# Kernel optimization log

Measured on AMD Instinct MI355X. Metric: run time of the kernel, lower is better.

## Reference

```python
import jax, jax.numpy as jnp
import numpy as np

N_NODES = 50000
IN_FEATS, HID_FEATS, OUT_FEATS, HEADS = 128, 32, 64, 4
NEG_SLOPE = 0.2
EPS = 1e-16


def gat_conv(x, src, dst, W, att_src, att_dst, bias, heads, out_ch, concat):
    """PyG-style GATConv. src/dst: [E] (self-loops already included).
    W: [in, heads*out_ch]; att_src/att_dst: [heads, out_ch]; bias: [heads*out_ch] or [out_ch].
    """
    n = x.shape[0]
    xw = (x @ W).reshape(n, heads, out_ch)                     # [N,H,C]
    a_src = (xw * att_src).sum(-1)                             # [N,H]
    a_dst = (xw * att_dst).sum(-1)                             # [N,H]
    e = jax.nn.leaky_relu(a_src[src] + a_dst[dst], NEG_SLOPE)  # [E,H]
    # segment softmax over incoming edges of each destination node
    m = jax.ops.segment_max(e, dst, num_segments=n)
    e = jnp.exp(e - m[dst])
    denom = jax.ops.segment_sum(e, dst, num_segments=n)
    alpha = e / (denom[dst] + EPS)                             # [E,H]
    out = jax.ops.segment_sum(alpha[:, :, None] * xw[src], dst, num_segments=n)  # [N,H,C]
    out = out.reshape(n, heads * out_ch) if concat else out.mean(axis=1)
    return out + bias


def setup_inputs() -> dict:
    key = jax.random.key(0)
    ks = jax.random.split(key, 10)
    E = 1600000
    x = jax.random.normal(ks[0], (N_NODES, IN_FEATS), dtype=jnp.float32)
    edge_index = jax.random.randint(ks[1], (2, E), 0, N_NODES, dtype=jnp.int64)
    s1 = 1.0 / np.sqrt(IN_FEATS)
    W1 = jax.random.uniform(ks[2], (IN_FEATS, HEADS * HID_FEATS), jnp.float32, -s1, s1)
    att_src1 = jax.random.normal(ks[3], (HEADS, HID_FEATS), dtype=jnp.float32) * 0.1
    att_dst1 = jax.random.normal(ks[4], (HEADS, HID_FEATS), dtype=jnp.float32) * 0.1
    b1 = jnp.zeros((HEADS * HID_FEATS,), jnp.float32)
    s2 = 1.0 / np.sqrt(HEADS * HID_FEATS)
    W2 = jax.random.uniform(ks[5], (HEADS * HID_FEATS, OUT_FEATS), jnp.float32, -s2, s2)
    att_src2 = jax.random.normal(ks[6], (1, OUT_FEATS), dtype=jnp.float32) * 0.1
    att_dst2 = jax.random.normal(ks[7], (1, OUT_FEATS), dtype=jnp.float32) * 0.1
    b2 = jnp.zeros((OUT_FEATS,), jnp.float32)
    return {"x": x, "edge_index": edge_index, "W1": W1, "att_src1": att_src1,
            "att_dst1": att_dst1, "b1": b1, "W2": W2, "att_src2": att_src2,
            "att_dst2": att_dst2, "b2": b2}


def reference(x, edge_index, W1, att_src1, att_dst1, b1, W2, att_src2, att_dst2, b2):
    n = x.shape[0]
    loops = jnp.arange(n, dtype=edge_index.dtype)
    src = jnp.concatenate([edge_index[0], loops])
    dst = jnp.concatenate([edge_index[1], loops])
    h = gat_conv(x, src, dst, W1, att_src1, att_dst1, b1, HEADS, HID_FEATS, True)
    h = jax.nn.elu(h)
    h = gat_conv(h, src, dst, W2, att_src2, att_dst2, b2, 1, OUT_FEATS, False)
    return h.mean(axis=0)
```

## Files before the change

kernel.cpp:

```cpp
#include <hip/hip_runtime.h>
#include <math.h>

#define N_NODES 50000
#define SN      N_NODES
#define E_RAW   1600000
#define TE      (E_RAW + N_NODES)
#define TEP     (TE + 16 * N_NODES)
#define F_IN    128
#define H1      4
#define F1      128
#define F2      64
#define NEG_SLOPE 0.2f
#define EPS_F   1e-16f
#define XPAD    136
#define LOG2E   1.4426950408889634f

#define NBINS   196
#define NBLK_A  128
#define EPB     ((TE + NBLK_A - 1) / NBLK_A)
#define MM_BLOCKS (N_NODES / 16)

typedef float vf2 __attribute__((ext_vector_type(2)));
typedef short short8 __attribute__((ext_vector_type(8)));
typedef float f32x4 __attribute__((ext_vector_type(4)));

__device__ __forceinline__ unsigned short f2bf(float f) {
    unsigned u = __float_as_uint(f);
    return (unsigned short)((u + 0x7fffu + ((u >> 16) & 1u)) >> 16);
}
__device__ __forceinline__ unsigned char f2fp8(float f) {
    int p = __builtin_amdgcn_cvt_pk_fp8_f32(f, f, 0, false);
    return (unsigned char)(p & 0xff);
}
__device__ __forceinline__ vf2 fp8lo(unsigned u) {
    return __builtin_amdgcn_cvt_pk_f32_fp8((int)u, false);
}
__device__ __forceinline__ vf2 fp8hi(unsigned u) {
    return __builtin_amdgcn_cvt_pk_f32_fp8((int)u, true);
}
__device__ __forceinline__ vf2 pkfma(float w, vf2 a, vf2 c) {
#if __has_builtin(__builtin_elementwise_fma)
    vf2 wv = {w, w};
    return __builtin_elementwise_fma(wv, a, c);
#else
    c.x = fmaf(w, a.x, c.x);
    c.y = fmaf(w, a.y, c.y);
    return c;
#endif
}
__device__ __forceinline__ float fexp2(float x) {
#if __has_builtin(__builtin_amdgcn_exp2f)
    return __builtin_amdgcn_exp2f(x);
#else
    return exp2f(x);
#endif
}

__global__ __launch_bounds__(256) void k_prep(const float* __restrict__ W1,
                                              const float* __restrict__ W2,
                                              unsigned short* __restrict__ w1t,
                                              unsigned short* __restrict__ w2t,
                                              float* __restrict__ a1s,
                                              float* __restrict__ a2s,
                                              unsigned* __restrict__ xw1row,
                                              unsigned* __restrict__ xw2row) {
    int idx = blockIdx.x * 256 + threadIdx.x;
    if (idx < 16384) {
        int c = idx >> 7, k = idx & 127;
        w1t[idx] = f2bf(W1[k * F1 + c]);
    } else {
        int j = idx - 16384;
        int c = j >> 7, k = j & 127;
        w2t[j] = f2bf(W2[k * F2 + c]);
    }
    if (blockIdx.x == 0 && threadIdx.x < H1) a1s[SN * H1 + threadIdx.x] = -1e30f;
    if (blockIdx.x == 0 && threadIdx.x == H1) a2s[SN] = -1e30f;
    if (blockIdx.x == 1) {
        if (threadIdx.x < 32) xw1row[threadIdx.x] = 0u;
        else if (threadIdx.x < 48) xw2row[threadIdx.x - 32] = 0u;
    }
}

__global__ __launch_bounds__(256) void k_l1_mm_hist(
    const float* __restrict__ x, const unsigned short* __restrict__ w1t,
    const float* __restrict__ atts, const float* __restrict__ attd,
    unsigned char* __restrict__ xwf8, float* __restrict__ a1s, float* __restrict__ a1d,
    const int* __restrict__ ei, int* __restrict__ cnt) {
    __shared__ __align__(16) unsigned short wls[F1 * XPAD];
    __shared__ __align__(16) unsigned short xs[16 * XPAD];
    const int t = threadIdx.x;
    if (blockIdx.x >= MM_BLOCKS) {
        int* hist = (int*)wls;
        const int blk = blockIdx.x - MM_BLOCKS;
        for (int i = t; i < NBINS; i += 256) hist[i] = 0;
        __syncthreads();
        const int e0 = blk * EPB, e1 = min(TE, e0 + EPB);
        for (int e = e0 + t; e < e1; e += 256) {
            int d = (e < E_RAW) ? ei[E_RAW + e] : (e - E_RAW);
            atomicAdd(&hist[d >> 8], 1);
        }
        __syncthreads();
        for (int i = t; i < NBINS; i += 256) cnt[i * NBLK_A + blk] = hist[i];
        return;
    }
    const int n0 = blockIdx.x * 16;
    {
        const float4* src = (const float4*)(x + (size_t)n0 * F_IN);
#pragma unroll
        for (int i = 0; i < 2; ++i) {
            int idx = t + 256 * i;
            float4 v = src[idx];
            int row = idx >> 5;
            int col = (idx & 31) * 4;
            ushort4 o = { f2bf(v.x), f2bf(v.y), f2bf(v.z), f2bf(v.w) };
            *(ushort4*)(xs + row * XPAD + col) = o;
        }
        const uint4* wsrc = (const uint4*)w1t;
#pragma unroll
        for (int i = 0; i < 8; ++i) {
            int idx = t + 256 * i;
            uint4 v = wsrc[idx];
            int row = idx >> 4;
            int col = (idx & 15) * 8;
            *(uint4*)(wls + row * XPAD + col) = v;
        }
    }
    __syncthreads();
    const int w = t >> 6;
    const int lane = t & 63;
    const int quad = lane >> 4;
    const int ncol = lane & 15;
    const int ch0 = w * 32;
    const unsigned short* arow = xs + ncol * XPAD;
    const unsigned short* brow0 = wls + (ch0 + ncol) * XPAD;
    const unsigned short* brow1 = brow0 + 16 * XPAD;
    f32x4 acc0 = {0.f, 0.f, 0.f, 0.f}, acc1 = {0.f, 0.f, 0.f, 0.f};
#pragma unroll
    for (int s = 0; s < 4; ++s) {
        int kb = s * 32 + quad * 8;
        short8 a  = *(const short8*)(arow + kb);
        short8 b0 = *(const short8*)(brow0 + kb);
        short8 b1 = *(const short8*)(brow1 + kb);
        acc0 = __builtin_amdgcn_mfma_f32_16x16x32_bf16(a, b0, acc0, 0, 0, 0);
        acc1 = __builtin_amdgcn_mfma_f32_16x16x32_bf16(a, b1, acc1, 0, 0, 0);
    }
    const int ch = ch0 + ncol;
    const float as0 = atts[ch] * LOG2E, as1 = atts[ch + 16] * LOG2E;
    const float ad0 = attd[ch] * LOG2E, ad1 = attd[ch + 16] * LOG2E;
#pragma unroll
    for (int reg = 0; reg < 4; ++reg) {
        const int n = n0 + quad * 4 + reg;
        float v0 = acc0[reg], v1 = acc1[reg];
        xwf8[(size_t)n * F1 + ch] = f2fp8(v0);
        xwf8[(size_t)n * F1 + ch + 16] = f2fp8(v1);
        float ps = fmaf(v0, as0, v1 * as1);
        float pd = fmaf(v0, ad0, v1 * ad1);
#pragma unroll
        for (int off = 1; off < 16; off <<= 1) {
            ps += __shfl_xor(ps, off);
            pd += __shfl_xor(pd, off);
        }
        if (ncol == 0) {
            a1s[n * H1 + w] = ps;
            a1d[n * H1 + w] = pd;
        }
    }
}

__global__ __launch_bounds__(1024) void k_binscan(int* __restrict__ cnt,
                                                  int* __restrict__ bstart) {
    __shared__ int bt[NBINS];
    const int t = threadIdx.x, lane = t & 63, w = t >> 6;
    for (int bin = w; bin < NBINS; bin += 16) {
        int c0 = cnt[bin * NBLK_A + 2 * lane];
        int c1 = cnt[bin * NBLK_A + 2 * lane + 1];
        int s = c0 + c1;
        int incl = s;
#pragma unroll
        for (int off = 1; off < 64; off <<= 1) {
            int u = __shfl_up(incl, off, 64);
            if (lane >= off) incl += u;
        }
        int excl = incl - s;
        cnt[bin * NBLK_A + 2 * lane] = excl;
        cnt[bin * NBLK_A + 2 * lane + 1] = excl + c0;
        if (lane == 63) bt[bin] = incl;
    }
    __syncthreads();
    if (w == 0) {
        int v[4]; int s = 0;
#pragma unroll
        for (int j = 0; j < 4; ++j) {
            int i = 4 * lane + j;
            v[j] = (i < NBINS) ? bt[i] : 0;
            s += v[j];
        }
        int incl = s;
#pragma unroll
        for (int off = 1; off < 64; off <<= 1) {
            int u = __shfl_up(incl, off, 64);
            if (lane >= off) incl += u;
        }
        int run = incl - s;
#pragma unroll
        for (int j = 0; j < 4; ++j) {
            int i = 4 * lane + j;
            if (i < NBINS) bstart[i] = run;
            run += v[j];
        }
        if (lane == 63) bstart[NBINS] = TE;
    }
}

__global__ __launch_bounds__(256) void k_scatter_coarse(const int* __restrict__ ei,
                                                        const int* __restrict__ cnt,
                                                        const int* __restrict__ bstart,
                                                        unsigned* __restrict__ cbuf) {
    __shared__ int cur[NBINS];
    const int t = threadIdx.x, blk = blockIdx.x;
    for (int i = t; i < NBINS; i += 256) cur[i] = cnt[i * NBLK_A + blk] + bstart[i];
    __syncthreads();
    const int e0 = blk * EPB, e1 = min(TE, e0 + EPB);
    for (int e = e0 + t; e < e1; e += 256) {
        int s, d;
        if (e < E_RAW) { s = ei[e]; d = ei[E_RAW + e]; }
        else { s = e - E_RAW; d = s; }
        int pos = atomicAdd(&cur[d >> 8], 1);
        cbuf[pos] = ((unsigned)(d & 255) << 16) | (unsigned)s;
    }
}

__global__ __launch_bounds__(256) void k_fine_hist(const unsigned* __restrict__ cbuf,
                                                   const int* __restrict__ bstart,
                                                   int* __restrict__ deg) {
    __shared__ int hist[256];
    const int t = threadIdx.x, b = blockIdx.x;
    hist[t] = 0;
    __syncthreads();
    const int i0 = bstart[b], i1 = bstart[b + 1];
    for (int i = i0 + t; i < i1; i += 256) atomicAdd(&hist[cbuf[i] >> 16], 1);
    __syncthreads();
    const int d = b * 256 + t;
    if (d < N_NODES) deg[d] = hist[t];
}

__global__ __launch_bounds__(1024) void k_scan1(const int* __restrict__ deg,
                                                int* __restrict__ incl, int* __restrict__ bsum) {
    int t = threadIdx.x, g = blockIdx.x;
    int idx = g * 1024 + t;
    int v = (idx < N_NODES) ? ((deg[idx] + 15) & ~15) : 0;
    int lane = t & 63, w = t >> 6;
#pragma unroll
    for (int off = 1; off < 64; off <<= 1) {
        int u = __shfl_up(v, off, 64);
        if (lane >= off) v += u;
    }
    __shared__ int ws[16];
    if (lane == 63) ws[w] = v;
    __syncthreads();
    if (w == 0 && lane < 16) {
        int s = ws[lane];
#pragma unroll
        for (int off = 1; off < 16; off <<= 1) {
            int u = __shfl_up(s, off, 16);
            if (lane >= off) s += u;
        }
        ws[lane] = s;
    }
    __syncthreads();
    if (w > 0) v += ws[w - 1];
    if (idx < N_NODES) incl[idx] = v;
    if (t == 1023) bsum[g] = v;
}

__global__ __launch_bounds__(1024) void k_scan3(const int* __restrict__ incl,
                                                const int* __restrict__ bsum,
                                                int* __restrict__ rowstart) {
    __shared__ int soff;
    const int t = threadIdx.x;
    if (t < 64) {
        int v = (t < blockIdx.x) ? bsum[t] : 0;
#pragma unroll
        for (int off = 32; off >= 1; off >>= 1) v += __shfl_xor(v, off, 64);
        if (t == 0) soff = v;
    }
    __syncthreads();
    const int idx = blockIdx.x * 1024 + t;
    if (idx < N_NODES) rowstart[idx + 1] = incl[idx] + soff;
    if (idx == 0) rowstart[0] = 0;
}

__global__ __launch_bounds__(256) void k_build_csr(const unsigned* __restrict__ cbuf,
                                                   const int* __restrict__ bstart,
                                                   const int* __restrict__ rowstart,
                                                   const int* __restrict__ deg,
                                                   int* __restrict__ csr) {
    __shared__ int cur[256];
    const int t = threadIdx.x, b = blockIdx.x;
    const int d = b * 256 + t;
    cur[t] = (d < N_NODES) ? rowstart[d] : 0;
    __syncthreads();
    const int i0 = bstart[b], i1 = bstart[b + 1];
    for (int i = i0 + t; i < i1; i += 256) {
        unsigned v = cbuf[i];
        int pos = atomicAdd(&cur[v >> 16], 1);
        csr[pos] = (int)(v & 0xffffu);
    }
    __syncthreads();
    if (d < N_NODES) {
        const int pend = rowstart[d] + ((deg[d] + 15) & ~15);
        for (int i = cur[t]; i < pend; ++i) csr[i] = SN;
    }
}

__global__ __launch_bounds__(256) void k_l1_gather(
    const int* __restrict__ rowstart, const int* __restrict__ csr,
    const int* __restrict__ deg, const float* __restrict__ a1s,
    const float* __restrict__ a1d, const unsigned* __restrict__ xwu,
    const float* __restrict__ b1, float* __restrict__ h1) {
    const int lane = threadIdx.x & 63;
    const int wid = threadIdx.x >> 6;
    const int n = blockIdx.x * 4 + wid;
    if (n >= N_NODES) return;
    const int rs = rowstart[n];
    const int nb16 = (deg[n] + 15) >> 4;
    const int half = lane >> 5;
    const int sub = lane & 31;
    const int h = sub >> 3;
    const float adh = a1d[n * H1 + h];
    const int4* c4 = (const int4*)(csr + rs);
    const int eoff = half * 8 + (sub & 7);
    const int wbase = half * 32 + (h << 3);
    vf2 f01 = {0.f, 0.f}, f23 = {0.f, 0.f};
    float den_l = 0.f;
    for (int b = 0; b < nb16; ++b) {
        const int i0 = 4 * b + 2 * half;
        int4 sA = c4[i0], sB = c4[i0 + 1];
        int se = csr[rs + 16 * b + eoff];
        unsigned u0 = xwu[sA.x * 32 + sub], u1 = xwu[sA.y * 32 + sub];
        unsigned u2 = xwu[sA.z * 32 + sub], u3 = xwu[sA.w * 32 + sub];
        unsigned u4 = xwu[sB.x * 32 + sub], u5 = xwu[sB.y * 32 + sub];
        unsigned u6 = xwu[sB.z * 32 + sub], u7 = xwu[sB.w * 32 + sub];
        float sv = a1s[se * H1 + h] + adh;
        float we = fexp2(fmaxf(sv, NEG_SLOPE * sv));
        den_l += we;
        float w0 = __shfl(we, wbase + 0), w1 = __shfl(we, wbase + 1);
        float w2 = __shfl(we, wbase + 2), w3 = __shfl(we, wbase + 3);
        float w4 = __shfl(we, wbase + 4), w5 = __shfl(we, wbase + 5);
        float w6 = __shfl(we, wbase + 6), w7 = __shfl(we, wbase + 7);
        f01 = pkfma(w0, fp8lo(u0), f01); f23 = pkfma(w0, fp8hi(u0), f23);
        f01 = pkfma(w1, fp8lo(u1), f01); f23 = pkfma(w1, fp8hi(u1), f23);
        f01 = pkfma(w2, fp8lo(u2), f01); f23 = pkfma(w2, fp8hi(u2), f23);
        f01 = pkfma(w3, fp8lo(u3), f01); f23 = pkfma(w3, fp8hi(u3), f23);
        f01 = pkfma(w4, fp8lo(u4), f01); f23 = pkfma(w4, fp8hi(u4), f23);
        f01 = pkfma(w5, fp8lo(u5), f01); f23 = pkfma(w5, fp8hi(u5), f23);
        f01 = pkfma(w6, fp8lo(u6), f01); f23 = pkfma(w6, fp8hi(u6), f23);
        f01 = pkfma(w7, fp8lo(u7), f01); f23 = pkfma(w7, fp8hi(u7), f23);
    }
    float f0 = f01.x, f1 = f01.y, f2v = f23.x, f3 = f23.y;
    f0 += __shfl_xor(f0, 32);
    f1 += __shfl_xor(f1, 32);
    f2v += __shfl_xor(f2v, 32);
    f3 += __shfl_xor(f3, 32);
    den_l += __shfl_xor(den_l, 1);
    den_l += __shfl_xor(den_l, 2);
    den_l += __shfl_xor(den_l, 4);
    den_l += __shfl_xor(den_l, 32);
    if (half == 0) {
        const float inv = 1.f / (den_l + EPS_F);
        float4 bb = ((const float4*)b1)[sub];
        float o0 = fmaf(f0, inv, bb.x);
        float o1 = fmaf(f1, inv, bb.y);
        float o2 = fmaf(f2v, inv, bb.z);
        float o3 = fmaf(f3, inv, bb.w);
        o0 = o0 > 0.f ? o0 : expm1f(o0);
        o1 = o1 > 0.f ? o1 : expm1f(o1);
        o2 = o2 > 0.f ? o2 : expm1f(o2);
        o3 = o3 > 0.f ? o3 : expm1f(o3);
        ((float4*)h1)[(size_t)n * 32 + sub] = make_float4(o0, o1, o2, o3);
    }
}

__global__ __launch_bounds__(256) void k_l2_mm(
    const float* __restrict__ h1, const unsigned short* __restrict__ w2t,
    const float* __restrict__ atts, const float* __restrict__ attd,
    unsigned char* __restrict__ xwf8, float* __restrict__ a2s, float* __restrict__ a2d) {
    __shared__ __align__(16) unsigned short wls[F2 * XPAD];
    __shared__ __align__(16) unsigned short xs[16 * XPAD];
    __shared__ float parts[16][4], partd[16][4];
    const int t = threadIdx.x;
    const int n0 = blockIdx.x * 16;
    {
        const float4* src = (const float4*)(h1 + (size_t)n0 * F1);
#pragma unroll
        for (int i = 0; i < 2; ++i) {
            int idx = t + 256 * i;
            float4 v = src[idx];
            int row = idx >> 5;
            int col = (idx & 31) * 4;
            ushort4 o = { f2bf(v.x), f2bf(v.y), f2bf(v.z), f2bf(v.w) };
            *(ushort4*)(xs + row * XPAD + col) = o;
        }
        const uint4* wsrc = (const uint4*)w2t;
#pragma unroll
        for (int i = 0; i < 4; ++i) {
            int idx = t + 256 * i;
            uint4 v = wsrc[idx];
            int row = idx >> 4;
            int col = (idx & 15) * 8;
            *(uint4*)(wls + row * XPAD + col) = v;
        }
    }
    __syncthreads();
    const int w = t >> 6;
    const int lane = t & 63;
    const int quad = lane >> 4;
    const int ncol = lane & 15;
    const int ch0 = w * 16;
    const unsigned short* arow = xs + ncol * XPAD;
    const unsigned short* brow = wls + (ch0 + ncol) * XPAD;
    f32x4 acc = {0.f, 0.f, 0.f, 0.f};
#pragma unroll
    for (int s = 0; s < 4; ++s) {
        int kb = s * 32 + quad * 8;
        short8 a = *(const short8*)(arow + kb);
        short8 b = *(const short8*)(brow + kb);
        acc = __builtin_amdgcn_mfma_f32_16x16x32_bf16(a, b, acc, 0, 0, 0);
    }
    const int ch = ch0 + ncol;
    const float asv = atts[ch] * LOG2E, adv = attd[ch] * LOG2E;
#pragma unroll
    for (int reg = 0; reg < 4; ++reg) {
        const int m = quad * 4 + reg;
        float v = acc[reg];
        xwf8[(size_t)(n0 + m) * F2 + ch] = f2fp8(v);
        float ps = v * asv, pd = v * adv;
#pragma unroll
        for (int off = 1; off < 16; off <<= 1) {
            ps += __shfl_xor(ps, off);
            pd += __shfl_xor(pd, off);
        }
        if (ncol == 0) { parts[m][w] = ps; partd[m][w] = pd; }
    }
    __syncthreads();
    if (t < 16) {
        a2s[n0 + t] = (parts[t][0] + parts[t][1]) + (parts[t][2] + parts[t][3]);
        a2d[n0 + t] = (partd[t][0] + partd[t][1]) + (partd[t][2] + partd[t][3]);
    }
}

__global__ __launch_bounds__(256) void k_l2_gather(
    const int* __restrict__ rowstart, const int* __restrict__ csr,
    const int* __restrict__ deg, const float* __restrict__ a2s,
    const float* __restrict__ a2d, const unsigned* __restrict__ xwu,
    float* __restrict__ h2) {
    const int lane = threadIdx.x & 63;
    const int wid = threadIdx.x >> 6;
    const int n = blockIdx.x * 4 + wid;
    if (n >= N_NODES) return;
    const int rs = rowstart[n];
    const int nb16 = (deg[n] + 15) >> 4;
    const int q = lane >> 4;
    const int sub = lane & 15;
    const float adv = a2d[n];
    const int4* c4 = (const int4*)(csr + rs);
    vf2 f01 = {0.f, 0.f}, f23 = {0.f, 0.f};
    float den_l = 0.f;
    for (int b = 0; b < nb16; ++b) {
        int4 s4 = c4[4 * b + q];
        int se = csr[rs + 16 * b + sub];
        unsigned u0 = xwu[s4.x * 16 + sub], u1 = xwu[s4.y * 16 + sub];
        unsigned u2 = xwu[s4.z * 16 + sub], u3 = xwu[s4.w * 16 + sub];
        float sv = a2s[se] + adv;
        float we = fexp2(fmaxf(sv, NEG_SLOPE * sv));
        den_l += we;
        float w0 = __shfl(we, 4 * q + 0), w1 = __shfl(we, 4 * q + 1);
        float w2 = __shfl(we, 4 * q + 2), w3 = __shfl(we, 4 * q + 3);
        f01 = pkfma(w0, fp8lo(u0), f01); f23 = pkfma(w0, fp8hi(u0), f23);
        f01 = pkfma(w1, fp8lo(u1), f01); f23 = pkfma(w1, fp8hi(u1), f23);
        f01 = pkfma(w2, fp8lo(u2), f01); f23 = pkfma(w2, fp8hi(u2), f23);
        f01 = pkfma(w3, fp8lo(u3), f01); f23 = pkfma(w3, fp8hi(u3), f23);
    }
    float f0 = f01.x, f1 = f01.y, f2v = f23.x, f3 = f23.y;
#pragma unroll
    for (int off = 16; off <= 32; off <<= 1) {
        f0 += __shfl_xor(f0, off);
        f1 += __shfl_xor(f1, off);
        f2v += __shfl_xor(f2v, off);
        f3 += __shfl_xor(f3, off);
    }
#pragma unroll
    for (int off = 1; off <= 32; off <<= 1) den_l += __shfl_xor(den_l, off);
    if (lane < 16) {
        const float inv = 1.f / (0.25f * den_l + EPS_F);
        ((float4*)h2)[(size_t)n * 16 + sub] =
            make_float4(f0 * inv, f1 * inv, f2v * inv, f3 * inv);
    }
}

#define MEAN_BLOCKS 256
__global__ __launch_bounds__(256) void k_mean(const float* __restrict__ h2,
                                              double* __restrict__ accum) {
    const int t = threadIdx.x;
    const int c = t & 63;
    double acc = 0.0;
    const size_t total = (size_t)N_NODES * F2;
    for (size_t idx = (size_t)blockIdx.x * 256 + t; idx < total; idx += (size_t)MEAN_BLOCKS * 256)
        acc += (double)h2[idx];
    __shared__ double red[256];
    red[t] = acc;
    __syncthreads();
    if (t < 64) {
        double v = red[t] + red[t + 64] + red[t + 128] + red[t + 192];
        atomicAdd(&accum[c], v);
    }
}

__global__ void k_final(const double* __restrict__ accum, const float* __restrict__ b2,
                        float* __restrict__ out) {
    int t = threadIdx.x;
    if (t < F2) out[t] = (float)(accum[t] * (1.0 / (double)N_NODES)) + b2[t];
}

extern "C" void kernel_launch(void* const* d_in, const int* in_sizes, int n_in,
                              void* d_out, int out_size, void* d_ws, size_t ws_size,
                              hipStream_t stream) {
    (void)in_sizes; (void)n_in; (void)out_size; (void)ws_size;
    const float* x   = (const float*)d_in[0];
    const int*   ei  = (const int*)d_in[1];
    const float* W1  = (const float*)d_in[2];
    const float* as1 = (const float*)d_in[3];
    const float* ad1 = (const float*)d_in[4];
    const float* b1  = (const float*)d_in[5];
    const float* W2  = (const float*)d_in[6];
    const float* as2 = (const float*)d_in[7];
    const float* ad2 = (const float*)d_in[8];
    const float* b2  = (const float*)d_in[9];
    float* out = (float*)d_out;

    char* ws = (char*)d_ws;
    size_t off = 0;
    auto alloc = [&](size_t bytes) -> void* {
        void* p = ws + off;
        off += (bytes + 255) & ~(size_t)255;
        return p;
    };
    unsigned char*  xw1f8 = (unsigned char*)alloc((size_t)(N_NODES + 1) * F1);
    float* h1       = (float*)alloc((size_t)N_NODES * F1 * 4);
    unsigned char*  xw2f8 = (unsigned char*)alloc((size_t)(N_NODES + 1) * F2);
    float* h2       = (float*)alloc((size_t)N_NODES * F2 * 4);
    unsigned short* w1t = (unsigned short*)alloc((size_t)F1 * F1 * 2);
    unsigned short* w2t = (unsigned short*)alloc((size_t)F2 * F1 * 2);
    float* a1s      = (float*)alloc((size_t)(N_NODES + 1) * H1 * 4);
    float* a1d      = (float*)alloc((size_t)N_NODES * H1 * 4);
    float* a2s      = (float*)alloc((size_t)(N_NODES + 1) * 4);
    float* a2d      = (float*)alloc((size_t)N_NODES * 4);
    int*   deg      = (int*)alloc((size_t)N_NODES * 4);
    unsigned* cbuf  = (unsigned*)alloc((size_t)TE * 4);
    int*   cnt      = (int*)alloc((size_t)NBINS * NBLK_A * 4);
    int*   bstart   = (int*)alloc((size_t)(NBINS + 1) * 4);
    int*   rowstart = (int*)alloc((size_t)(N_NODES + 1) * 4);
    int*   csr      = (int*)alloc((size_t)TEP * 4);
    int*   incl     = (int*)alloc((size_t)N_NODES * 4);
    int*   bsum     = (int*)alloc(64 * 4);
    double* accum   = (double*)alloc(F2 * 8);

    const int nscan = (N_NODES + 1023) / 1024;
    const int nwave4 = (N_NODES + 3) / 4;

    hipMemsetAsync(accum, 0, F2 * 8, stream);
    k_prep<<<96, 256, 0, stream>>>(W1, W2, w1t, w2t, a1s, a2s,
                                   (unsigned*)(xw1f8 + (size_t)SN * F1),
                                   (unsigned*)(xw2f8 + (size_t)SN * F2));
    k_l1_mm_hist<<<MM_BLOCKS + NBLK_A, 256, 0, stream>>>(x, w1t, as1, ad1, xw1f8, a1s, a1d, ei, cnt);
    k_binscan<<<1, 1024, 0, stream>>>(cnt, bstart);
    k_scatter_coarse<<<NBLK_A, 256, 0, stream>>>(ei, cnt, bstart, cbuf);
    k_fine_hist<<<NBINS, 256, 0, stream>>>(cbuf, bstart, deg);
    k_scan1<<<nscan, 1024, 0, stream>>>(deg, incl, bsum);
    k_scan3<<<nscan, 1024, 0, stream>>>(incl, bsum, rowstart);
    k_build_csr<<<NBINS, 256, 0, stream>>>(cbuf, bstart, rowstart, deg, csr);
    k_l1_gather<<<nwave4, 256, 0, stream>>>(rowstart, csr, deg, a1s, a1d,
                                            (const unsigned*)xw1f8, b1, h1);
    k_l2_mm<<<MM_BLOCKS, 256, 0, stream>>>(h1, w2t, as2, ad2, xw2f8, a2s, a2d);
    k_l2_gather<<<nwave4, 256, 0, stream>>>(rowstart, csr, deg, a2s, a2d,
                                            (const unsigned*)xw2f8, h2);
    k_mean<<<MEAN_BLOCKS, 256, 0, stream>>>(h2, accum);
    k_final<<<1, 64, 0, stream>>>(accum, b2, out);
}
```

Measured before the change: 274.0 us.

## Compute gather attention weights once per edge into LDS, split bin scan

The layer-1 and layer-2 gather kernels now compute each edge's attention weight a single time per 128-slot chunk, covering all heads with one float4 load in layer 1, and stage the weights in shared memory. The old code recomputed the exponentials redundantly across lanes and broadcast them with shuffles. This removes duplicated exp work and shuffle traffic, at the cost of LDS writes and reads and an extra chunk loop. It also splits the single-block bin scan into a 196-block per-bin scan plus a small one-wave kernel, which adds a kernel launch in exchange for more parallelism.

After: 278.3 us. No clear change (+1.6%).

```diff
diff --git a/kernel.cpp b/kernel.cpp
--- a/kernel.cpp
+++ b/kernel.cpp
@@ -14,6 +14,7 @@
 #define EPS_F   1e-16f
 #define XPAD    136
 #define LOG2E   1.4426950408889634f
+#define NB16_MAX (TEP / 16)
 
 #define NBINS   196
 #define NBLK_A  128
@@ -167,49 +168,47 @@
     }
 }
 
-__global__ __launch_bounds__(1024) void k_binscan(int* __restrict__ cnt,
-                                                  int* __restrict__ bstart) {
-    __shared__ int bt[NBINS];
-    const int t = threadIdx.x, lane = t & 63, w = t >> 6;
-    for (int bin = w; bin < NBINS; bin += 16) {
-        int c0 = cnt[bin * NBLK_A + 2 * lane];
-        int c1 = cnt[bin * NBLK_A + 2 * lane + 1];
-        int s = c0 + c1;
-        int incl = s;
-#pragma unroll
-        for (int off = 1; off < 64; off <<= 1) {
-            int u = __shfl_up(incl, off, 64);
-            if (lane >= off) incl += u;
-        }
-        int excl = incl - s;
-        cnt[bin * NBLK_A + 2 * lane] = excl;
-        cnt[bin * NBLK_A + 2 * lane + 1] = excl + c0;
-        if (lane == 63) bt[bin] = incl;
-    }
-    __syncthreads();
-    if (w == 0) {
-        int v[4]; int s = 0;
-#pragma unroll
-        for (int j = 0; j < 4; ++j) {
-            int i = 4 * lane + j;
-            v[j] = (i < NBINS) ? bt[i] : 0;
-            s += v[j];
-        }
-        int incl = s;
-#pragma unroll
-        for (int off = 1; off < 64; off <<= 1) {
-            int u = __shfl_up(incl, off, 64);
-            if (lane >= off) incl += u;
-        }
-        int run = incl - s;
-#pragma unroll
-        for (int j = 0; j < 4; ++j) {
-            int i = 4 * lane + j;
-            if (i < NBINS) bstart[i] = run;
-            run += v[j];
-        }
-        if (lane == 63) bstart[NBINS] = TE;
-    }
+__global__ __launch_bounds__(64) void k_btot(int* __restrict__ cnt, int* __restrict__ btot) {
+    const int bin = blockIdx.x, lane = threadIdx.x;
+    int c0 = cnt[bin * NBLK_A + 2 * lane];
+    int c1 = cnt[bin * NBLK_A + 2 * lane + 1];
+    int s = c0 + c1;
+    int incl = s;
+#pragma unroll
+    for (int off = 1; off < 64; off <<= 1) {
+        int u = __shfl_up(incl, off, 64);
+        if (lane >= off) incl += u;
+    }
+    int excl = incl - s;
+    cnt[bin * NBLK_A + 2 * lane] = excl;
+    cnt[bin * NBLK_A + 2 * lane + 1] = excl + c0;
+    if (lane == 63) btot[bin] = incl;
+}
+
+__global__ __launch_bounds__(64) void k_bstart(const int* __restrict__ btot,
+                                               int* __restrict__ bstart) {
+    const int lane = threadIdx.x;
+    int v[4]; int s = 0;
+#pragma unroll
+    for (int j = 0; j < 4; ++j) {
+        int i = 4 * lane + j;
+        v[j] = (i < NBINS) ? btot[i] : 0;
+        s += v[j];
+    }
+    int incl = s;
+#pragma unroll
+    for (int off = 1; off < 64; off <<= 1) {
+        int u = __shfl_up(incl, off, 64);
+        if (lane >= off) incl += u;
+    }
+    int run = incl - s;
+#pragma unroll
+    for (int j = 0; j < 4; ++j) {
+        int i = 4 * lane + j;
+        if (i < NBINS) bstart[i] = run;
+        run += v[j];
+    }
+    if (lane == 63) bstart[NBINS] = TE;
 }
 
 __global__ __launch_bounds__(256) void k_scatter_coarse(const int* __restrict__ ei,
@@ -318,53 +317,67 @@
     const int* __restrict__ deg, const float* __restrict__ a1s,
     const float* __restrict__ a1d, const unsigned* __restrict__ xwu,
     const float* __restrict__ b1, float* __restrict__ h1) {
+    __shared__ float wlds[4][128 * 4];
     const int lane = threadIdx.x & 63;
     const int wid = threadIdx.x >> 6;
     const int n = blockIdx.x * 4 + wid;
     if (n >= N_NODES) return;
     const int rs = rowstart[n];
-    const int nb16 = (deg[n] + 15) >> 4;
+    const int nb16 = min((deg[n] + 15) >> 4, NB16_MAX);
+    const int nslots = nb16 << 4;
     const int half = lane >> 5;
     const int sub = lane & 31;
     const int h = sub >> 3;
-    const float adh = a1d[n * H1 + h];
+    float* wl = wlds[wid];
     const int4* c4 = (const int4*)(csr + rs);
-    const int eoff = half * 8 + (sub & 7);
-    const int wbase = half * 32 + (h << 3);
+    const float4 ad4 = *(const float4*)(a1d + n * H1);
     vf2 f01 = {0.f, 0.f}, f23 = {0.f, 0.f};
     float den_l = 0.f;
-    for (int b = 0; b < nb16; ++b) {
-        const int i0 = 4 * b + 2 * half;
-        int4 sA = c4[i0], sB = c4[i0 + 1];
-        int se = csr[rs + 16 * b + eoff];
-        unsigned u0 = xwu[sA.x * 32 + sub], u1 = xwu[sA.y * 32 + sub];
-        unsigned u2 = xwu[sA.z * 32 + sub], u3 = xwu[sA.w * 32 + sub];
-        unsigned u4 = xwu[sB.x * 32 + sub], u5 = xwu[sB.y * 32 + sub];
-        unsigned u6 = xwu[sB.z * 32 + sub], u7 = xwu[sB.w * 32 + sub];
-        float sv = a1s[se * H1 + h] + adh;
-        float we = fexp2(fmaxf(sv, NEG_SLOPE * sv));
-        den_l += we;
-        float w0 = __shfl(we, wbase + 0), w1 = __shfl(we, wbase + 1);
-        float w2 = __shfl(we, wbase + 2), w3 = __shfl(we, wbase + 3);
-        float w4 = __shfl(we, wbase + 4), w5 = __shfl(we, wbase + 5);
-        float w6 = __shfl(we, wbase + 6), w7 = __shfl(we, wbase + 7);
-        f01 = pkfma(w0, fp8lo(u0), f01); f23 = pkfma(w0, fp8hi(u0), f23);
-        f01 = pkfma(w1, fp8lo(u1), f01); f23 = pkfma(w1, fp8hi(u1), f23);
-        f01 = pkfma(w2, fp8lo(u2), f01); f23 = pkfma(w2, fp8hi(u2), f23);
-        f01 = pkfma(w3, fp8lo(u3), f01); f23 = pkfma(w3, fp8hi(u3), f23);
-        f01 = pkfma(w4, fp8lo(u4), f01); f23 = pkfma(w4, fp8hi(u4), f23);
-        f01 = pkfma(w5, fp8lo(u5), f01); f23 = pkfma(w5, fp8hi(u5), f23);
-        f01 = pkfma(w6, fp8lo(u6), f01); f23 = pkfma(w6, fp8hi(u6), f23);
-        f01 = pkfma(w7, fp8lo(u7), f01); f23 = pkfma(w7, fp8hi(u7), f23);
+    for (int c0 = 0; c0 < nslots; c0 += 128) {
+#pragma unroll
+        for (int rep = 0; rep < 2; ++rep) {
+            const int sl = (rep << 6) + lane;
+            const int s = c0 + sl;
+            float4 w4 = {0.f, 0.f, 0.f, 0.f};
+            if (s < nslots) {
+                const int src = csr[rs + s];
+                const float4 as4 = *(const float4*)(a1s + src * H1);
+                float v;
+                v = as4.x + ad4.x; w4.x = fexp2(fmaxf(v, NEG_SLOPE * v));
+                v = as4.y + ad4.y; w4.y = fexp2(fmaxf(v, NEG_SLOPE * v));
+                v = as4.z + ad4.z; w4.z = fexp2(fmaxf(v, NEG_SLOPE * v));
+                v = as4.w + ad4.w; w4.w = fexp2(fmaxf(v, NEG_SLOPE * v));
+            }
+            *(float4*)(wl + sl * 4) = w4;
+        }
+        const int b0 = c0 >> 4;
+        const int bend = min(nb16, b0 + 8);
+        for (int b = b0; b < bend; ++b) {
+            const int i0 = 4 * b + 2 * half;
+            const int4 sA = c4[i0], sB = c4[i0 + 1];
+            const float* wb = wl + (((b - b0) << 4) + (half << 3)) * 4 + h;
+            const float w0 = wb[0],  w1 = wb[4],  w2 = wb[8],  w3 = wb[12];
+            const float w4_ = wb[16], w5 = wb[20], w6 = wb[24], w7 = wb[28];
+            unsigned u0 = xwu[sA.x * 32 + sub], u1 = xwu[sA.y * 32 + sub];
+            unsigned u2 = xwu[sA.z * 32 + sub], u3 = xwu[sA.w * 32 + sub];
+            unsigned u4 = xwu[sB.x * 32 + sub], u5 = xwu[sB.y * 32 + sub];
+            unsigned u6 = xwu[sB.z * 32 + sub], u7 = xwu[sB.w * 32 + sub];
+            den_l += ((w0 + w1) + (w2 + w3)) + ((w4_ + w5) + (w6 + w7));
+            f01 = pkfma(w0, fp8lo(u0), f01); f23 = pkfma(w0, fp8hi(u0), f23);
+            f01 = pkfma(w1, fp8lo(u1), f01); f23 = pkfma(w1, fp8hi(u1), f23);
+            f01 = pkfma(w2, fp8lo(u2), f01); f23 = pkfma(w2, fp8hi(u2), f23);
+            f01 = pkfma(w3, fp8lo(u3), f01); f23 = pkfma(w3, fp8hi(u3), f23);
+            f01 = pkfma(w4_, fp8lo(u4), f01); f23 = pkfma(w4_, fp8hi(u4), f23);
+            f01 = pkfma(w5, fp8lo(u5), f01); f23 = pkfma(w5, fp8hi(u5), f23);
+            f01 = pkfma(w6, fp8lo(u6), f01); f23 = pkfma(w6, fp8hi(u6), f23);
+            f01 = pkfma(w7, fp8lo(u7), f01); f23 = pkfma(w7, fp8hi(u7), f23);
+        }
     }
     float f0 = f01.x, f1 = f01.y, f2v = f23.x, f3 = f23.y;
     f0 += __shfl_xor(f0, 32);
     f1 += __shfl_xor(f1, 32);
     f2v += __shfl_xor(f2v, 32);
     f3 += __shfl_xor(f3, 32);
-    den_l += __shfl_xor(den_l, 1);
-    den_l += __shfl_xor(den_l, 2);
-    den_l += __shfl_xor(den_l, 4);
     den_l += __shfl_xor(den_l, 32);
     if (half == 0) {
         const float inv = 1.f / (den_l + EPS_F);
@@ -454,32 +467,48 @@
     const int* __restrict__ deg, const float* __restrict__ a2s,
     const float* __restrict__ a2d, const unsigned* __restrict__ xwu,
     float* __restrict__ h2) {
+    __shared__ float wlds[4][128];
     const int lane = threadIdx.x & 63;
     const int wid = threadIdx.x >> 6;
     const int n = blockIdx.x * 4 + wid;
     if (n >= N_NODES) return;
     const int rs = rowstart[n];
-    const int nb16 = (deg[n] + 15) >> 4;
+    const int nb16 = min((deg[n] + 15) >> 4, NB16_MAX);
+    const int nslots = nb16 << 4;
     const int q = lane >> 4;
     const int sub = lane & 15;
+    float* wl = wlds[wid];
     const float adv = a2d[n];
     const int4* c4 = (const int4*)(csr + rs);
     vf2 f01 = {0.f, 0.f}, f23 = {0.f, 0.f};
     float den_l = 0.f;
-    for (int b = 0; b < nb16; ++b) {
-        int4 s4 = c4[4 * b + q];
-        int se = csr[rs + 16 * b + sub];
-        unsigned u0 = xwu[s4.x * 16 + sub], u1 = xwu[s4.y * 16 + sub];
-        unsigned u2 = xwu[s4.z * 16 + sub], u3 = xwu[s4.w * 16 + sub];
-        float sv = a2s[se] + adv;
-        float we = fexp2(fmaxf(sv, NEG_SLOPE * sv));
-        den_l += we;
-        float w0 = __shfl(we, 4 * q + 0), w1 = __shfl(we, 4 * q + 1);
-        float w2 = __shfl(we, 4 * q + 2), w3 = __shfl(we, 4 * q + 3);
-        f01 = pkfma(w0, fp8lo(u0), f01); f23 = pkfma(w0, fp8hi(u0), f23);
-        f01 = pkfma(w1, fp8lo(u1), f01); f23 = pkfma(w1, fp8hi(u1), f23);
-        f01 = pkfma(w2, fp8lo(u2), f01); f23 = pkfma(w2, fp8hi(u2), f23);
-        f01 = pkfma(w3, fp8lo(u3), f01); f23 = pkfma(w3, fp8hi(u3), f23);
+    for (int c0 = 0; c0 < nslots; c0 += 128) {
+#pragma unroll
+        for (int rep = 0; rep < 2; ++rep) {
+            const int sl = (rep << 6) + lane;
+            const int s = c0 + sl;
+            float wv = 0.f;
+            if (s < nslots) {
+                const int src = csr[rs + s];
+                const float v = a2s[src] + adv;
+                wv = fexp2(fmaxf(v, NEG_SLOPE * v));
+            }
+            wl[sl] = wv;
+        }
+        const int b0 = c0 >> 4;
+        const int bend = min(nb16, b0 + 8);
+        for (int b = b0; b < bend; ++b) {
+            const int4 s4 = c4[4 * b + q];
+            const float* wb = wl + ((b - b0) << 4) + (q << 2);
+            const float w0 = wb[0], w1 = wb[1], w2 = wb[2], w3 = wb[3];
+            unsigned u0 = xwu[s4.x * 16 + sub], u1 = xwu[s4.y * 16 + sub];
+            unsigned u2 = xwu[s4.z * 16 + sub], u3 = xwu[s4.w * 16 + sub];
+            den_l += (w0 + w1) + (w2 + w3);
+            f01 = pkfma(w0, fp8lo(u0), f01); f23 = pkfma(w0, fp8hi(u0), f23);
+            f01 = pkfma(w1, fp8lo(u1), f01); f23 = pkfma(w1, fp8hi(u1), f23);
+            f01 = pkfma(w2, fp8lo(u2), f01); f23 = pkfma(w2, fp8hi(u2), f23);
+            f01 = pkfma(w3, fp8lo(u3), f01); f23 = pkfma(w3, fp8hi(u3), f23);
+        }
     }
     float f0 = f01.x, f1 = f01.y, f2v = f23.x, f3 = f23.y;
 #pragma unroll
@@ -488,11 +517,10 @@
         f1 += __shfl_xor(f1, off);
         f2v += __shfl_xor(f2v, off);
         f3 += __shfl_xor(f3, off);
-    }
-#pragma unroll
-    for (int off = 1; off <= 32; off <<= 1) den_l += __shfl_xor(den_l, off);
+        den_l += __shfl_xor(den_l, off);
+    }
     if (lane < 16) {
-        const float inv = 1.f / (0.25f * den_l + EPS_F);
+        const float inv = 1.f / (den_l + EPS_F);
         ((float4*)h2)[(size_t)n * 16 + sub] =
             make_float4(f0 * inv, f1 * inv, f2v * inv, f3 * inv);
     }
@@ -558,6 +586,7 @@
     int*   deg      = (int*)alloc((size_t)N_NODES * 4);
     unsigned* cbuf  = (unsigned*)alloc((size_t)TE * 4);
     int*   cnt      = (int*)alloc((size_t)NBINS * NBLK_A * 4);
+    int*   btot     = (int*)alloc((size_t)NBINS * 4);
     int*   bstart   = (int*)alloc((size_t)(NBINS + 1) * 4);
     int*   rowstart = (int*)alloc((size_t)(N_NODES + 1) * 4);
     int*   csr      = (int*)alloc((size_t)TEP * 4);
@@ -573,7 +602,8 @@
                                    (unsigned*)(xw1f8 + (size_t)SN * F1),
                                    (unsigned*)(xw2f8 + (size_t)SN * F2));
     k_l1_mm_hist<<<MM_BLOCKS + NBLK_A, 256, 0, stream>>>(x, w1t, as1, ad1, xw1f8, a1s, a1d, ei, cnt);
-    k_binscan<<<1, 1024, 0, stream>>>(cnt, bstart);
+    k_btot<<<NBINS, 64, 0, stream>>>(cnt, btot);
+    k_bstart<<<1, 64, 0, stream>>>(btot, bstart);
     k_scatter_coarse<<<NBLK_A, 256, 0, stream>>>(ei, cnt, bstart, cbuf);
     k_fine_hist<<<NBINS, 256, 0, stream>>>(cbuf, bstart, deg);
     k_scan1<<<nscan, 1024, 0, stream>>>(deg, incl, bsum);
```

## Replace two-level binned CSR build with global-atomic degree count and direct scatter

Applied to the files above, without the earlier changes.

Drops the coarse-bin histogram, bin scan, coarse scatter, fine histogram and CSR build kernels. Degrees are now counted with global atomics on each destination node, padding is filled during the scan, and edges are scattered straight into the CSR through per-node atomic cursors. This removes three kernel launches and the intermediate cbuf pass, at the cost of heavily contended global atomics over random destinations and less-local scattered writes. Edge order within each row becomes nondeterministic.

After: 408.0 us. 48.9% more time.

```diff
diff --git a/kernel.cpp b/kernel.cpp
--- a/kernel.cpp
+++ b/kernel.cpp
@@ -14,11 +14,12 @@
 #define EPS_F   1e-16f
 #define XPAD    136
 #define LOG2E   1.4426950408889634f
-
-#define NBINS   196
+#define NB16_MAX (TEP / 16)
+
 #define NBLK_A  128
 #define EPB     ((TE + NBLK_A - 1) / NBLK_A)
 #define MM_BLOCKS (N_NODES / 16)
+#define SC_BLOCKS 2048
 
 typedef float vf2 __attribute__((ext_vector_type(2)));
 typedef short short8 __attribute__((ext_vector_type(8)));
@@ -85,22 +86,17 @@
     const float* __restrict__ x, const unsigned short* __restrict__ w1t,
     const float* __restrict__ atts, const float* __restrict__ attd,
     unsigned char* __restrict__ xwf8, float* __restrict__ a1s, float* __restrict__ a1d,
-    const int* __restrict__ ei, int* __restrict__ cnt) {
+    const int* __restrict__ ei, int* __restrict__ deg) {
     __shared__ __align__(16) unsigned short wls[F1 * XPAD];
     __shared__ __align__(16) unsigned short xs[16 * XPAD];
     const int t = threadIdx.x;
     if (blockIdx.x >= MM_BLOCKS) {
-        int* hist = (int*)wls;
         const int blk = blockIdx.x - MM_BLOCKS;
-        for (int i = t; i < NBINS; i += 256) hist[i] = 0;
-        __syncthreads();
         const int e0 = blk * EPB, e1 = min(TE, e0 + EPB);
         for (int e = e0 + t; e < e1; e += 256) {
             int d = (e < E_RAW) ? ei[E_RAW + e] : (e - E_RAW);
-            atomicAdd(&hist[d >> 8], 1);
-        }
-        __syncthreads();
-        for (int i = t; i < NBINS; i += 256) cnt[i * NBLK_A + blk] = hist[i];
+            atomicAdd(&deg[d], 1);
+        }
         return;
     }
     const int n0 = blockIdx.x * 16;
@@ -167,83 +163,6 @@
     }
 }
 
-__global__ __launch_bounds__(1024) void k_binscan(int* __restrict__ cnt,
-                                                  int* __restrict__ bstart) {
-    __shared__ int bt[NBINS];
-    const int t = threadIdx.x, lane = t & 63, w = t >> 6;
-    for (int bin = w; bin < NBINS; bin += 16) {
-        int c0 = cnt[bin * NBLK_A + 2 * lane];
-        int c1 = cnt[bin * NBLK_A + 2 * lane + 1];
-        int s = c0 + c1;
-        int incl = s;
-#pragma unroll
-        for (int off = 1; off < 64; off <<= 1) {
-            int u = __shfl_up(incl, off, 64);
-            if (lane >= off) incl += u;
-        }
-        int excl = incl - s;
-        cnt[bin * NBLK_A + 2 * lane] = excl;
-        cnt[bin * NBLK_A + 2 * lane + 1] = excl + c0;
-        if (lane == 63) bt[bin] = incl;
-    }
-    __syncthreads();
-    if (w == 0) {
-        int v[4]; int s = 0;
-#pragma unroll
-        for (int j = 0; j < 4; ++j) {
-            int i = 4 * lane + j;
-            v[j] = (i < NBINS) ? bt[i] : 0;
-            s += v[j];
-        }
-        int incl = s;
-#pragma unroll
-        for (int off = 1; off < 64; off <<= 1) {
-            int u = __shfl_up(incl, off, 64);
-            if (lane >= off) incl += u;
-        }
-        int run = incl - s;
-#pragma unroll
-        for (int j = 0; j < 4; ++j) {
-            int i = 4 * lane + j;
-            if (i < NBINS) bstart[i] = run;
-            run += v[j];
-        }
-        if (lane == 63) bstart[NBINS] = TE;
-    }
-}
-
-__global__ __launch_bounds__(256) void k_scatter_coarse(const int* __restrict__ ei,
-                                                        const int* __restrict__ cnt,
-                                                        const int* __restrict__ bstart,
-                                                        unsigned* __restrict__ cbuf) {
-    __shared__ int cur[NBINS];
-    const int t = threadIdx.x, blk = blockIdx.x;
-    for (int i = t; i < NBINS; i += 256) cur[i] = cnt[i * NBLK_A + blk] + bstart[i];
-    __syncthreads();
-    const int e0 = blk * EPB, e1 = min(TE, e0 + EPB);
-    for (int e = e0 + t; e < e1; e += 256) {
-        int s, d;
-        if (e < E_RAW) { s = ei[e]; d = ei[E_RAW + e]; }
-        else { s = e - E_RAW; d = s; }
-        int pos = atomicAdd(&cur[d >> 8], 1);
-        cbuf[pos] = ((unsigned)(d & 255) << 16) | (unsigned)s;
-    }
-}
-
-__global__ __launch_bounds__(256) void k_fine_hist(const unsigned* __restrict__ cbuf,
-                                                   const int* __restrict__ bstart,
-                                                   int* __restrict__ deg) {
-    __shared__ int hist[256];
-    const int t = threadIdx.x, b = blockIdx.x;
-    hist[t] = 0;
-    __syncthreads();
-    const int i0 = bstart[b], i1 = bstart[b + 1];
-    for (int i = i0 + t; i < i1; i += 256) atomicAdd(&hist[cbuf[i] >> 16], 1);
-    __syncthreads();
-    const int d = b * 256 + t;
-    if (d < N_NODES) deg[d] = hist[t];
-}
-
 __global__ __launch_bounds__(1024) void k_scan1(const int* __restrict__ deg,
                                                 int* __restrict__ incl, int* __restrict__ bsum) {
     int t = threadIdx.x, g = blockIdx.x;
@@ -275,7 +194,10 @@
 
 __global__ __launch_bounds__(1024) void k_scan3(const int* __restrict__ incl,
                                                 const int* __restrict__ bsum,
-                                                int* __restrict__ rowstart) {
+                                                const int* __restrict__ deg,
+                                                int* __restrict__ rowstart,
+                                                int* __restrict__ cur,
+                                                int* __restrict__ csr) {
     __shared__ int soff;
     const int t = threadIdx.x;
     if (t < 64) {
@@ -286,30 +208,26 @@
     }
     __syncthreads();
     const int idx = blockIdx.x * 1024 + t;
-    if (idx < N_NODES) rowstart[idx + 1] = incl[idx] + soff;
+    if (idx < N_NODES) {
+        const int rend = incl[idx] + soff;
+        rowstart[idx + 1] = rend;
+        const int d = deg[idx];
+        const int rbeg = rend - ((d + 15) & ~15);
+        cur[idx] = rbeg;
+        for (int i = rbeg + d; i < rend; ++i) csr[i] = SN;
+    }
     if (idx == 0) rowstart[0] = 0;
 }
 
-__global__ __launch_bounds__(256) void k_build_csr(const unsigned* __restrict__ cbuf,
-                                                   const int* __restrict__ bstart,
-                                                   const int* __restrict__ rowstart,
-                                                   const int* __restrict__ deg,
-                                                   int* __restrict__ csr) {
-    __shared__ int cur[256];
-    const int t = threadIdx.x, b = blockIdx.x;
-    const int d = b * 256 + t;
-    cur[t] = (d < N_NODES) ? rowstart[d] : 0;
-    __syncthreads();
-    const int i0 = bstart[b], i1 = bstart[b + 1];
-    for (int i = i0 + t; i < i1; i += 256) {
-        unsigned v = cbuf[i];
-        int pos = atomicAdd(&cur[v >> 16], 1);
-        csr[pos] = (int)(v & 0xffffu);
-    }
-    __syncthreads();
-    if (d < N_NODES) {
-        const int pend = rowstart[d] + ((deg[d] + 15) & ~15);
-        for (int i = cur[t]; i < pend; ++i) csr[i] = SN;
+__global__ __launch_bounds__(256) void k_scatter_direct(const int* __restrict__ ei,
+                                                        int* __restrict__ cur,
+                                                        int* __restrict__ csr) {
+    for (int e = blockIdx.x * 256 + threadIdx.x; e < TE; e += SC_BLOCKS * 256) {
+        int s, d;
+        if (e < E_RAW) { s = ei[e]; d = ei[E_RAW + e]; }
+        else { s = e - E_RAW; d = s; }
+        int pos = atomicAdd(&cur[d], 1);
+        csr[pos] = s;
     }
 }
 
@@ -323,7 +241,7 @@
     const int n = blockIdx.x * 4 + wid;
     if (n >= N_NODES) return;
     const int rs = rowstart[n];
-    const int nb16 = (deg[n] + 15) >> 4;
+    const int nb16 = min((deg[n] + 15) >> 4, NB16_MAX);
     const int half = lane >> 5;
     const int sub = lane & 31;
     const int h = sub >> 3;
@@ -459,7 +377,7 @@
     const int n = blockIdx.x * 4 + wid;
     if (n >= N_NODES) return;
     const int rs = rowstart[n];
-    const int nb16 = (deg[n] + 15) >> 4;
+    const int nb16 = min((deg[n] + 15) >> 4, NB16_MAX);
     const int q = lane >> 4;
     const int sub = lane & 15;
     const float adv = a2d[n];
@@ -545,6 +463,8 @@
         off += (bytes + 255) & ~(size_t)255;
         return p;
     };
+    double* accum   = (double*)alloc(F2 * 8);
+    int*   deg      = (int*)alloc((size_t)N_NODES * 4);
     unsigned char*  xw1f8 = (unsigned char*)alloc((size_t)(N_NODES + 1) * F1);
     float* h1       = (float*)alloc((size_t)N_NODES * F1 * 4);
     unsigned char*  xw2f8 = (unsigned char*)alloc((size_t)(N_NODES + 1) * F2);
@@ -555,30 +475,23 @@
     float* a1d      = (float*)alloc((size_t)N_NODES * H1 * 4);
     float* a2s      = (float*)alloc((size_t)(N_NODES + 1) * 4);
     float* a2d      = (float*)alloc((size_t)N_NODES * 4);
-    int*   deg      = (int*)alloc((size_t)N_NODES * 4);
-    unsigned* cbuf  = (unsigned*)alloc((size_t)TE * 4);
-    int*   cnt      = (int*)alloc((size_t)NBINS * NBLK_A * 4);
-    int*   bstart   = (int*)alloc((size_t)(NBINS + 1) * 4);
     int*   rowstart = (int*)alloc((size_t)(N_NODES + 1) * 4);
+    int*   cur      = (int*)alloc((size_t)N_NODES * 4);
     int*   csr      = (int*)alloc((size_t)TEP * 4);
     int*   incl     = (int*)alloc((size_t)N_NODES * 4);
     int*   bsum     = (int*)alloc(64 * 4);
-    double* accum   = (double*)alloc(F2 * 8);
 
     const int nscan = (N_NODES + 1023) / 1024;
     const int nwave4 = (N_NODES + 3) / 4;
 
-    hipMemsetAsync(accum, 0, F2 * 8, stream);
+    hipMemsetAsync(accum, 0, 512 + (size_t)N_NODES * 4, stream);
     k_prep<<<96, 256, 0, stream>>>(W1, W2, w1t, w2t, a1s, a2s,
                                    (unsigned*)(xw1f8 + (size_t)SN * F1),
                                    (unsigned*)(xw2f8 + (size_t)SN * F2));
-    k_l1_mm_hist<<<MM_BLOCKS + NBLK_A, 256, 0, stream>>>(x, w1t, as1, ad1, xw1f8, a1s, a1d, ei, cnt);
-    k_binscan<<<1, 1024, 0, stream>>>(cnt, bstart);
-    k_scatter_coarse<<<NBLK_A, 256, 0, stream>>>(ei, cnt, bstart, cbuf);
-    k_fine_hist<<<NBINS, 256, 0, stream>>>(cbuf, bstart, deg);
+    k_l1_mm_hist<<<MM_BLOCKS + NBLK_A, 256, 0, stream>>>(x, w1t, as1, ad1, xw1f8, a1s, a1d, ei, deg);
     k_scan1<<<nscan, 1024, 0, stream>>>(deg, incl, bsum);
-    k_scan3<<<nscan, 1024, 0, stream>>>(incl, bsum, rowstart);
-    k_build_csr<<<NBINS, 256, 0, stream>>>(cbuf, bstart, rowstart, deg, csr);
+    k_scan3<<<nscan, 1024, 0, stream>>>(incl, bsum, deg, rowstart, cur, csr);
+    k_scatter_direct<<<SC_BLOCKS, 256, 0, stream>>>(ei, cur, csr);
     k_l1_gather<<<nwave4, 256, 0, stream>>>(rowstart, csr, deg, a1s, a1d,
                                             (const unsigned*)xw1f8, b1, h1);
     k_l2_mm<<<MM_BLOCKS, 256, 0, stream>>>(h1, w2t, as2, ad2, xw2f8, a2s, a2d);
```
